# Kernel tuning notes

Measured on AMD Instinct MI355X. Metric: run time of the kernel, lower is better.

The kernel has to match this reference:

```python
import jax, jax.numpy as jnp
import numpy as np

N = 50000          # nodes
E = 800000         # edges (avg degree 16)
FEATS = [96, 96, 96, 48]


def setup_inputs() -> dict:
    key = jax.random.key(0)
    ks = jax.random.split(key, 10)
    x = jax.random.normal(ks[0], (N, FEATS[0]), dtype=jnp.float32)
    edge_index = jax.random.randint(ks[1], (2, E), 0, N, dtype=jnp.int64)
    d = {"x": x, "edge_index": edge_index}
    i = 2
    for l in range(3):
        s = 1.0 / np.sqrt(FEATS[l])
        d[f"Wl{l}"] = jax.random.uniform(ks[i], (FEATS[l], FEATS[l + 1]), jnp.float32, -s, s); i += 1
        d[f"Wr{l}"] = jax.random.uniform(ks[i], (FEATS[l], FEATS[l + 1]), jnp.float32, -s, s); i += 1
        d[f"b{l}"] = jnp.zeros((FEATS[l + 1],), jnp.float32)
    return d


def _sage_layer(h, src, dst, Wl, Wr, b, n):
    # PyG SAGEConv (aggr='mean', root_weight=True, normalize=False):
    # out_i = W_l @ mean_{j in N(i)} h_j + W_r @ h_i + b
    msg = h[src]                                                   # [E, F] gather
    ssum = jax.ops.segment_sum(msg, dst, num_segments=n)           # [N, F] scatter-add
    cnt = jax.ops.segment_sum(jnp.ones((src.shape[0], 1), h.dtype), dst, num_segments=n)
    mean = ssum / jnp.maximum(cnt, 1.0)
    return mean @ Wl + h @ Wr + b


def reference(x, edge_index, Wl0, Wr0, b0, Wl1, Wr1, b1, Wl2, Wr2, b2):
    src, dst = edge_index[0], edge_index[1]
    n = x.shape[0]
    # block = SAGEConv -> ReLU -> dropout(identity in eval)
    h = jax.nn.relu(_sage_layer(x, src, dst, Wl0, Wr0, b0, n))
    h = jax.nn.relu(_sage_layer(h, src, dst, Wl1, Wr1, b1, n))
    h = jax.nn.relu(_sage_layer(h, src, dst, Wl2, Wr2, b2, n))
    return h
```

## Files before the change

### kernel.cpp

```cpp
#include <hip/hip_runtime.h>


#define NNODES 50000
#define ZROW   50000
#define NEDGES 800000
#define CAP    64
#define LSTR   72
#define NBKT   512
#define BKSZ   98
#define NBKB   511
#define EBA    400
#define EPBA   2000
#define SEGC   20
#define CVT_N8 600000
#define CB 1172
#define WTN 46080
#define WB 90

typedef __attribute__((ext_vector_type(8))) short bf16x8;
typedef __attribute__((ext_vector_type(4))) float f32x4;

__device__ inline unsigned short f2bf(float f) {
    unsigned int u = __float_as_uint(f);
    unsigned int r = (u + 0x7fffu + ((u >> 16) & 1u)) >> 16;
    return (unsigned short)r;
}
__device__ inline float bf2f_lo(unsigned int u) { return __uint_as_float(u << 16); }
__device__ inline float bf2f_hi(unsigned int u) { return __uint_as_float(u & 0xffff0000u); }

__global__ __launch_bounds__(512) void build_a(
        const int* __restrict__ src, const int* __restrict__ dst,
        unsigned int* __restrict__ region, unsigned char* __restrict__ cnta,
        const float* __restrict__ x, unsigned short* __restrict__ h0b,
        const float* __restrict__ Wl0, const float* __restrict__ Wr0,
        const float* __restrict__ Wl1, const float* __restrict__ Wr1,
        const float* __restrict__ Wl2, const float* __restrict__ Wr2,
        unsigned short* __restrict__ WT0, unsigned short* __restrict__ WT1,
        unsigned short* __restrict__ WT2) {
    int b = blockIdx.x;
    if (b < EBA) {
        __shared__ int hist[NBKT];
        const int t = threadIdx.x;
        for (int k = t; k < NBKT; k += 512) hist[k] = 0;
        __syncthreads();
        const int e0 = b * EPBA;
        for (int i = t; i < EPBA; i += 512) {
            int d = dst[e0 + i];
            int s = src[e0 + i];
            unsigned int bk = (unsigned int)d / 98u;
            unsigned int rel = (unsigned int)d - bk * 98u;
            unsigned int val = (rel << 16) | (unsigned int)s;
            int r = atomicAdd(&hist[bk], 1);
            if (r < SEGC) region[((size_t)b * NBKT + bk) * SEGC + r] = val;
        }
        __syncthreads();
        for (int k = t; k < NBKT; k += 512)
            cnta[(size_t)k * EBA + b] = (unsigned char)min(hist[k], SEGC);
    } else if (b < EBA + CB) {
        long long t = (long long)(b - EBA) * 512 + threadIdx.x;
        if (t < CVT_N8) {
            const float4* p = reinterpret_cast<const float4*>(x + t * 8);
            float4 a = p[0], c = p[1];
            uint4 o;
            o.x = (unsigned)f2bf(a.x) | ((unsigned)f2bf(a.y) << 16);
            o.y = (unsigned)f2bf(a.z) | ((unsigned)f2bf(a.w) << 16);
            o.z = (unsigned)f2bf(c.x) | ((unsigned)f2bf(c.y) << 16);
            o.w = (unsigned)f2bf(c.z) | ((unsigned)f2bf(c.w) << 16);
            *reinterpret_cast<uint4*>(h0b + t * 8) = o;
        }
    } else if (b < EBA + CB + WB) {
        int t = (b - EBA - CB) * 512 + threadIdx.x;
        if (t >= WTN) return;
        const float* Wl; const float* Wr; unsigned short* WT; int fout; int u;
        if (t < 18432)      { Wl = Wl0; Wr = Wr0; WT = WT0; fout = 96; u = t; }
        else if (t < 36864) { Wl = Wl1; Wr = Wr1; WT = WT1; fout = 96; u = t - 18432; }
        else                { Wl = Wl2; Wr = Wr2; WT = WT2; fout = 48; u = t - 36864; }
        int j = u / 192;
        int k = u - j * 192;
        float v = (k < 96) ? Wl[k * fout + j] : Wr[(k - 96) * fout + j];
        WT[u] = f2bf(v);
    } else {
        int t = threadIdx.x;
        if (t < 12) {
            uint4 z = make_uint4(0, 0, 0, 0);
            *reinterpret_cast<uint4*>(h0b + (size_t)ZROW * 96 + t * 8) = z;
        }
    }
}

__global__ __launch_bounds__(512) void build_b(const unsigned int* __restrict__ region,
                                               const unsigned char* __restrict__ cnta,
                                               int* __restrict__ deg,
                                               unsigned short* __restrict__ colu) {
    __shared__ unsigned char cnt_l[EBA];
    __shared__ int deg_l[BKSZ];
    __shared__ __attribute__((aligned(16))) unsigned short colu_l[BKSZ * CAP];
    const int k = blockIdx.x;
    const int t = threadIdx.x;
    const int base_node = k * BKSZ;
    const int nn = min(BKSZ, NNODES - base_node);
    for (int i = t; i < EBA; i += 512) cnt_l[i] = cnta[(size_t)k * EBA + i];
    if (t < BKSZ) deg_l[t] = 0;
    __syncthreads();

    for (int cb = t; cb < EBA; cb += 512) {
        const int c = cnt_l[cb];
        const unsigned int* cell = region + ((size_t)cb * NBKT + k) * SEGC;
        for (int j = 0; j < c; j += 4) {
            uint4 q = *reinterpret_cast<const uint4*>(cell + j);
            unsigned int qq0 = q.x, qq1 = q.y, qq2 = q.z, qq3 = q.w;
            if (j + 0 < c) {
                int local = (int)(qq0 >> 16);
                int r = atomicAdd(&deg_l[local], 1);
                if (r < CAP) colu_l[local * CAP + r] = (unsigned short)(qq0 & 0xffffu);
            }
            if (j + 1 < c) {
                int local = (int)(qq1 >> 16);
                int r = atomicAdd(&deg_l[local], 1);
                if (r < CAP) colu_l[local * CAP + r] = (unsigned short)(qq1 & 0xffffu);
            }
            if (j + 2 < c) {
                int local = (int)(qq2 >> 16);
                int r = atomicAdd(&deg_l[local], 1);
                if (r < CAP) colu_l[local * CAP + r] = (unsigned short)(qq2 & 0xffffu);
            }
            if (j + 3 < c) {
                int local = (int)(qq3 >> 16);
                int r = atomicAdd(&deg_l[local], 1);
                if (r < CAP) colu_l[local * CAP + r] = (unsigned short)(qq3 & 0xffffu);
            }
        }
    }
    __syncthreads();

    for (int i = t; i < nn * (CAP / 8); i += 512) {
        *reinterpret_cast<uint4*>(colu + (size_t)base_node * CAP + i * 8) =
            *reinterpret_cast<const uint4*>(colu_l + i * 8);
    }
    if (t < nn) deg[base_node + t] = deg_l[t];
}

template <int NT, bool WRITE_BF16>
__global__ __launch_bounds__(256) void fused_layer(
    const unsigned short* __restrict__ hb,
    const int* __restrict__ deg, const unsigned short* __restrict__ colu,
    const unsigned short* __restrict__ WT,
    const float* __restrict__ bias,
    unsigned short* __restrict__ out_bf, float* __restrict__ out_f) {
    __shared__ unsigned short Asm[16][200];
    __shared__ unsigned short cols[16 * LSTR];
    const int i0 = blockIdx.x * 16;
    const int t = threadIdx.x;

    if (WRITE_BF16 && blockIdx.x == 0 && t < 12) {
        uint4 z = make_uint4(0, 0, 0, 0);
        *reinterpret_cast<uint4*>(out_bf + (size_t)ZROW * 96 + t * 8) = z;
    }

    {
        int u4 = t * 4;
        int node = u4 >> 6;
        int slot = u4 & 63;
        uint2 v = *reinterpret_cast<const uint2*>(colu + (size_t)(i0 + node) * CAP + slot);
        int d = deg[i0 + node];
        unsigned int s0 = (slot + 0 < d) ? (v.x & 0xffffu) : ZROW;
        unsigned int s1 = (slot + 1 < d) ? (v.x >> 16)     : ZROW;
        unsigned int s2 = (slot + 2 < d) ? (v.y & 0xffffu) : ZROW;
        unsigned int s3 = (slot + 3 < d) ? (v.y >> 16)     : ZROW;
        uint2 o;
        o.x = s0 | (s1 << 16);
        o.y = s2 | (s3 << 16);
        *reinterpret_cast<uint2*>(&cols[node * LSTR + slot]) = o;
    }
    __syncthreads();

    if (t < 192) {
        const int nl = t / 12;
        const int c = (t - nl * 12) * 8;
        const int d = deg[i0 + nl];
        const int d8 = d & ~7;
        const int pd4 = (d + 3) & ~3;
        float a0 = 0.f, a1 = 0.f, a2 = 0.f, a3 = 0.f, a4 = 0.f, a5 = 0.f, a6 = 0.f, a7 = 0.f;
        int j = 0;
        for (; j < d8; j += 8) {
            uint4 cu = *reinterpret_cast<const uint4*>(&cols[nl * LSTR + j]);
            int s0 = (int)(cu.x & 0xffffu), s1 = (int)(cu.x >> 16);
            int s2 = (int)(cu.y & 0xffffu), s3 = (int)(cu.y >> 16);
            int s4 = (int)(cu.z & 0xffffu), s5 = (int)(cu.z >> 16);
            int s6 = (int)(cu.w & 0xffffu), s7 = (int)(cu.w >> 16);
            uint4 u0 = *reinterpret_cast<const uint4*>(hb + (size_t)s0 * 96 + c);
            uint4 u1 = *reinterpret_cast<const uint4*>(hb + (size_t)s1 * 96 + c);
            uint4 u2 = *reinterpret_cast<const uint4*>(hb + (size_t)s2 * 96 + c);
            uint4 u3 = *reinterpret_cast<const uint4*>(hb + (size_t)s3 * 96 + c);
            uint4 u4 = *reinterpret_cast<const uint4*>(hb + (size_t)s4 * 96 + c);
            uint4 u5 = *reinterpret_cast<const uint4*>(hb + (size_t)s5 * 96 + c);
            uint4 u6 = *reinterpret_cast<const uint4*>(hb + (size_t)s6 * 96 + c);
            uint4 u7 = *reinterpret_cast<const uint4*>(hb + (size_t)s7 * 96 + c);
            a0 += bf2f_lo(u0.x) + bf2f_lo(u1.x) + bf2f_lo(u2.x) + bf2f_lo(u3.x)
                + bf2f_lo(u4.x) + bf2f_lo(u5.x) + bf2f_lo(u6.x) + bf2f_lo(u7.x);
            a1 += bf2f_hi(u0.x) + bf2f_hi(u1.x) + bf2f_hi(u2.x) + bf2f_hi(u3.x)
                + bf2f_hi(u4.x) + bf2f_hi(u5.x) + bf2f_hi(u6.x) + bf2f_hi(u7.x);
            a2 += bf2f_lo(u0.y) + bf2f_lo(u1.y) + bf2f_lo(u2.y) + bf2f_lo(u3.y)
                + bf2f_lo(u4.y) + bf2f_lo(u5.y) + bf2f_lo(u6.y) + bf2f_lo(u7.y);
            a3 += bf2f_hi(u0.y) + bf2f_hi(u1.y) + bf2f_hi(u2.y) + bf2f_hi(u3.y)
                + bf2f_hi(u4.y) + bf2f_hi(u5.y) + bf2f_hi(u6.y) + bf2f_hi(u7.y);
            a4 += bf2f_lo(u0.z) + bf2f_lo(u1.z) + bf2f_lo(u2.z) + bf2f_lo(u3.z)
                + bf2f_lo(u4.z) + bf2f_lo(u5.z) + bf2f_lo(u6.z) + bf2f_lo(u7.z);
            a5 += bf2f_hi(u0.z) + bf2f_hi(u1.z) + bf2f_hi(u2.z) + bf2f_hi(u3.z)
                + bf2f_hi(u4.z) + bf2f_hi(u5.z) + bf2f_hi(u6.z) + bf2f_hi(u7.z);
            a6 += bf2f_lo(u0.w) + bf2f_lo(u1.w) + bf2f_lo(u2.w) + bf2f_lo(u3.w)
                + bf2f_lo(u4.w) + bf2f_lo(u5.w) + bf2f_lo(u6.w) + bf2f_lo(u7.w);
            a7 += bf2f_hi(u0.w) + bf2f_hi(u1.w) + bf2f_hi(u2.w) + bf2f_hi(u3.w)
                + bf2f_hi(u4.w) + bf2f_hi(u5.w) + bf2f_hi(u6.w) + bf2f_hi(u7.w);
        }
        for (; j < pd4; j += 4) {
            uint2 cu = *reinterpret_cast<const uint2*>(&cols[nl * LSTR + j]);
            int s0 = (int)(cu.x & 0xffffu), s1 = (int)(cu.x >> 16);
            int s2 = (int)(cu.y & 0xffffu), s3 = (int)(cu.y >> 16);
            uint4 u0 = *reinterpret_cast<const uint4*>(hb + (size_t)s0 * 96 + c);
            uint4 u1 = *reinterpret_cast<const uint4*>(hb + (size_t)s1 * 96 + c);
            uint4 u2 = *reinterpret_cast<const uint4*>(hb + (size_t)s2 * 96 + c);
            uint4 u3 = *reinterpret_cast<const uint4*>(hb + (size_t)s3 * 96 + c);
            a0 += bf2f_lo(u0.x) + bf2f_lo(u1.x) + bf2f_lo(u2.x) + bf2f_lo(u3.x);
            a1 += bf2f_hi(u0.x) + bf2f_hi(u1.x) + bf2f_hi(u2.x) + bf2f_hi(u3.x);
            a2 += bf2f_lo(u0.y) + bf2f_lo(u1.y) + bf2f_lo(u2.y) + bf2f_lo(u3.y);
            a3 += bf2f_hi(u0.y) + bf2f_hi(u1.y) + bf2f_hi(u2.y) + bf2f_hi(u3.y);
            a4 += bf2f_lo(u0.z) + bf2f_lo(u1.z) + bf2f_lo(u2.z) + bf2f_lo(u3.z);
            a5 += bf2f_hi(u0.z) + bf2f_hi(u1.z) + bf2f_hi(u2.z) + bf2f_hi(u3.z);
            a6 += bf2f_lo(u0.w) + bf2f_lo(u1.w) + bf2f_lo(u2.w) + bf2f_lo(u3.w);
            a7 += bf2f_hi(u0.w) + bf2f_hi(u1.w) + bf2f_hi(u2.w) + bf2f_hi(u3.w);
        }
        float inv = (d > 0) ? 1.0f / (float)d : 0.0f;
        uint4 o;
        o.x = (unsigned)f2bf(a0 * inv) | ((unsigned)f2bf(a1 * inv) << 16);
        o.y = (unsigned)f2bf(a2 * inv) | ((unsigned)f2bf(a3 * inv) << 16);
        o.z = (unsigned)f2bf(a4 * inv) | ((unsigned)f2bf(a5 * inv) << 16);
        o.w = (unsigned)f2bf(a6 * inv) | ((unsigned)f2bf(a7 * inv) << 16);
        *reinterpret_cast<uint4*>(&Asm[nl][c]) = o;
    }
    __syncthreads();

    const int wave = t >> 6;
    const int lane = t & 63;
    const int m = lane & 15;
    const int kq = (lane >> 4) * 8;

    bf16x8 afr[6];
#pragma unroll
    for (int kk = 0; kk < 3; ++kk)
        afr[kk] = *reinterpret_cast<const bf16x8*>(&Asm[m][kq + kk * 32]);
    const unsigned short* hrow = hb + (size_t)(i0 + m) * 96 + kq;
#pragma unroll
    for (int kk = 0; kk < 3; ++kk)
        afr[3 + kk] = *reinterpret_cast<const bf16x8*>(hrow + kk * 32);

    const int r0 = (lane >> 4) * 4;
    for (int nt = wave; nt < NT; nt += 4) {
        f32x4 acc = {0.f, 0.f, 0.f, 0.f};
        const unsigned short* wrow = WT + (size_t)(nt * 16 + m) * 192 + kq;
#pragma unroll
        for (int kk = 0; kk < 6; ++kk) {
            bf16x8 bfr = *reinterpret_cast<const bf16x8*>(wrow + kk * 32);
            acc = __builtin_amdgcn_mfma_f32_16x16x32_bf16(afr[kk], bfr, acc, 0, 0, 0);
        }
        int colj = nt * 16 + m;
        float bv = bias[colj];
#pragma unroll
        for (int r = 0; r < 4; ++r) {
            float v = fmaxf(acc[r] + bv, 0.0f);
            size_t oi = (size_t)(i0 + r0 + r) * (16 * NT) + colj;
            if (WRITE_BF16) out_bf[oi] = f2bf(v);
            else            out_f[oi] = v;
        }
    }
}

extern "C" void kernel_launch(void* const* d_in, const int* in_sizes, int n_in,
                              void* d_out, int out_size, void* d_ws, size_t ws_size,
                              hipStream_t stream) {
    const float* x   = (const float*)d_in[0];
    const int*   ei  = (const int*)d_in[1];
    const float* Wl0 = (const float*)d_in[2];
    const float* Wr0 = (const float*)d_in[3];
    const float* b0  = (const float*)d_in[4];
    const float* Wl1 = (const float*)d_in[5];
    const float* Wr1 = (const float*)d_in[6];
    const float* b1  = (const float*)d_in[7];
    const float* Wl2 = (const float*)d_in[8];
    const float* Wr2 = (const float*)d_in[9];
    const float* b2  = (const float*)d_in[10];
    float* out = (float*)d_out;

    const int* src = ei;
    const int* dst = ei + NEDGES;

    char* p = (char*)d_ws;
    int* deg = (int*)p;                        p += (size_t)50176 * 4;
    unsigned short* colu = (unsigned short*)p; p += (size_t)50176 * CAP * 2;
    unsigned char* cnta = (unsigned char*)p;   p += (size_t)NBKT * EBA;
    unsigned short* WT0 = (unsigned short*)p;  p += 96 * 192 * 2;
    unsigned short* WT1 = (unsigned short*)p;  p += 96 * 192 * 2;
    unsigned short* WT2 = (unsigned short*)p;  p += 48 * 192 * 2;
    unsigned short* h0b = (unsigned short*)p;  p += (size_t)(NNODES + 1) * 96 * 2 + 64;
    unsigned short* h1b = (unsigned short*)p;  p += (size_t)(NNODES + 1) * 96 * 2 + 64;
    unsigned short* h2b = (unsigned short*)p;  p += (size_t)(NNODES + 1) * 96 * 2 + 64;

    unsigned int* region = (unsigned int*)h1b;

    build_a<<<EBA + CB + WB + 1, 512, 0, stream>>>(
        src, dst, region, cnta, x, h0b,
        Wl0, Wr0, Wl1, Wr1, Wl2, Wr2, WT0, WT1, WT2);

    build_b<<<NBKB, 512, 0, stream>>>(region, cnta, deg, colu);

    const int LB = NNODES / 16;
    fused_layer<6, true><<<LB, 256, 0, stream>>>(h0b, deg, colu, WT0, b0, h1b, nullptr);
    fused_layer<6, true><<<LB, 256, 0, stream>>>(h1b, deg, colu, WT1, b1, h2b, nullptr);
    fused_layer<3, false><<<LB, 256, 0, stream>>>(h2b, deg, colu, WT2, b2, nullptr, out);
}
```

Measured before the change: 195.4 us.

## Project last layer before aggregation to gather 48-wide features instead of 96

Uses linearity of mean aggregation to apply Wl2 to h2 inside the layer-1 epilogue, writing a 48-wide bf16 Y2 array. The final kernel then gathers and averages the narrower projected features and adds the root term plus bias. This halves gather traffic in the last layer. In exchange it adds an extra barrier and a small MFMA in layer 1, and the projected values are rounded to bf16 before averaging.

```diff
diff --git a/kernel.cpp b/kernel.cpp
--- a/kernel.cpp
+++ b/kernel.cpp
@@ -36,7 +36,7 @@
         const float* __restrict__ Wl1, const float* __restrict__ Wr1,
         const float* __restrict__ Wl2, const float* __restrict__ Wr2,
         unsigned short* __restrict__ WT0, unsigned short* __restrict__ WT1,
-        unsigned short* __restrict__ WT2) {
+        unsigned short* __restrict__ WT2l, unsigned short* __restrict__ WT2r) {
     int b = blockIdx.x;
     if (b < EBA) {
         __shared__ int hist[NBKT];
@@ -71,14 +71,21 @@
     } else if (b < EBA + CB + WB) {
         int t = (b - EBA - CB) * 512 + threadIdx.x;
         if (t >= WTN) return;
-        const float* Wl; const float* Wr; unsigned short* WT; int fout; int u;
-        if (t < 18432)      { Wl = Wl0; Wr = Wr0; WT = WT0; fout = 96; u = t; }
-        else if (t < 36864) { Wl = Wl1; Wr = Wr1; WT = WT1; fout = 96; u = t - 18432; }
-        else                { Wl = Wl2; Wr = Wr2; WT = WT2; fout = 48; u = t - 36864; }
-        int j = u / 192;
-        int k = u - j * 192;
-        float v = (k < 96) ? Wl[k * fout + j] : Wr[(k - 96) * fout + j];
-        WT[u] = f2bf(v);
+        if (t < 18432) {
+            int u = t; int j = u / 192; int k = u - j * 192;
+            float v = (k < 96) ? Wl0[k * 96 + j] : Wr0[(k - 96) * 96 + j];
+            WT0[u] = f2bf(v);
+        } else if (t < 36864) {
+            int u = t - 18432; int j = u / 192; int k = u - j * 192;
+            float v = (k < 96) ? Wl1[k * 96 + j] : Wr1[(k - 96) * 96 + j];
+            WT1[u] = f2bf(v);
+        } else if (t < 41472) {
+            int u = t - 36864; int j = u / 96; int k = u - j * 96;
+            WT2l[u] = f2bf(Wl2[k * 48 + j]);
+        } else {
+            int u = t - 41472; int j = u / 96; int k = u - j * 96;
+            WT2r[u] = f2bf(Wr2[k * 48 + j]);
+        }
     } else {
         int t = threadIdx.x;
         if (t < 12) {
@@ -140,21 +147,29 @@
     if (t < nn) deg[base_node + t] = deg_l[t];
 }
 
-template <int NT, bool WRITE_BF16>
+template <int NT, bool Y2EP>
 __global__ __launch_bounds__(256) void fused_layer(
     const unsigned short* __restrict__ hb,
     const int* __restrict__ deg, const unsigned short* __restrict__ colu,
     const unsigned short* __restrict__ WT,
     const float* __restrict__ bias,
-    unsigned short* __restrict__ out_bf, float* __restrict__ out_f) {
+    unsigned short* __restrict__ out_bf,
+    const unsigned short* __restrict__ WT2l,
+    unsigned short* __restrict__ Y2b) {
     __shared__ unsigned short Asm[16][200];
     __shared__ unsigned short cols[16 * LSTR];
     const int i0 = blockIdx.x * 16;
     const int t = threadIdx.x;
 
-    if (WRITE_BF16 && blockIdx.x == 0 && t < 12) {
-        uint4 z = make_uint4(0, 0, 0, 0);
-        *reinterpret_cast<uint4*>(out_bf + (size_t)ZROW * 96 + t * 8) = z;
+    if (blockIdx.x == 0) {
+        if (t < 12) {
+            uint4 z = make_uint4(0, 0, 0, 0);
+            *reinterpret_cast<uint4*>(out_bf + (size_t)ZROW * 96 + t * 8) = z;
+        }
+        if (Y2EP && t >= 16 && t < 22) {
+            uint4 z = make_uint4(0, 0, 0, 0);
+            *reinterpret_cast<uint4*>(Y2b + (size_t)ZROW * 48 + (t - 16) * 8) = z;
+        }
     }
 
     {
@@ -254,6 +269,8 @@
     for (int kk = 0; kk < 3; ++kk)
         afr[3 + kk] = *reinterpret_cast<const bf16x8*>(hrow + kk * 32);
 
+    if (Y2EP) __syncthreads();
+
     const int r0 = (lane >> 4) * 4;
     for (int nt = wave; nt < NT; nt += 4) {
         f32x4 acc = {0.f, 0.f, 0.f, 0.f};
@@ -268,9 +285,153 @@
 #pragma unroll
         for (int r = 0; r < 4; ++r) {
             float v = fmaxf(acc[r] + bv, 0.0f);
-            size_t oi = (size_t)(i0 + r0 + r) * (16 * NT) + colj;
-            if (WRITE_BF16) out_bf[oi] = f2bf(v);
-            else            out_f[oi] = v;
+            unsigned short hv = f2bf(v);
+            out_bf[(size_t)(i0 + r0 + r) * (16 * NT) + colj] = hv;
+            if (Y2EP) Asm[r0 + r][colj] = hv;
+        }
+    }
+
+    if (Y2EP) {
+        __syncthreads();
+        if (wave < 3) {
+            bf16x8 a2[3];
+#pragma unroll
+            for (int kk = 0; kk < 3; ++kk)
+                a2[kk] = *reinterpret_cast<const bf16x8*>(&Asm[m][kq + kk * 32]);
+            f32x4 acc = {0.f, 0.f, 0.f, 0.f};
+            const unsigned short* wrow = WT2l + (size_t)(wave * 16 + m) * 96 + kq;
+#pragma unroll
+            for (int kk = 0; kk < 3; ++kk) {
+                bf16x8 bfr = *reinterpret_cast<const bf16x8*>(wrow + kk * 32);
+                acc = __builtin_amdgcn_mfma_f32_16x16x32_bf16(a2[kk], bfr, acc, 0, 0, 0);
+            }
+            int colj2 = wave * 16 + m;
+#pragma unroll
+            for (int r = 0; r < 4; ++r)
+                Y2b[(size_t)(i0 + r0 + r) * 48 + colj2] = f2bf(acc[r]);
+        }
+    }
+}
+
+__global__ __launch_bounds__(256) void fused_final(
+    const unsigned short* __restrict__ hb,
+    const unsigned short* __restrict__ Y2b,
+    const int* __restrict__ deg, const unsigned short* __restrict__ colu,
+    const unsigned short* __restrict__ WT2r,
+    const float* __restrict__ bias,
+    float* __restrict__ out_f) {
+    __shared__ float Msm[16][56];
+    __shared__ unsigned short cols[16 * LSTR];
+    const int i0 = blockIdx.x * 16;
+    const int t = threadIdx.x;
+
+    {
+        int u4 = t * 4;
+        int node = u4 >> 6;
+        int slot = u4 & 63;
+        uint2 v = *reinterpret_cast<const uint2*>(colu + (size_t)(i0 + node) * CAP + slot);
+        int d = deg[i0 + node];
+        unsigned int s0 = (slot + 0 < d) ? (v.x & 0xffffu) : ZROW;
+        unsigned int s1 = (slot + 1 < d) ? (v.x >> 16)     : ZROW;
+        unsigned int s2 = (slot + 2 < d) ? (v.y & 0xffffu) : ZROW;
+        unsigned int s3 = (slot + 3 < d) ? (v.y >> 16)     : ZROW;
+        uint2 o;
+        o.x = s0 | (s1 << 16);
+        o.y = s2 | (s3 << 16);
+        *reinterpret_cast<uint2*>(&cols[node * LSTR + slot]) = o;
+    }
+    __syncthreads();
+
+    if (t < 96) {
+        const int nl = t / 6;
+        const int c = (t - nl * 6) * 8;
+        const int d = deg[i0 + nl];
+        const int d8 = d & ~7;
+        const int pd4 = (d + 3) & ~3;
+        float a0 = 0.f, a1 = 0.f, a2 = 0.f, a3 = 0.f, a4 = 0.f, a5 = 0.f, a6 = 0.f, a7 = 0.f;
+        int j = 0;
+        for (; j < d8; j += 8) {
+            uint4 cu = *reinterpret_cast<const uint4*>(&cols[nl * LSTR + j]);
+            int s0 = (int)(cu.x & 0xffffu), s1 = (int)(cu.x >> 16);
+            int s2 = (int)(cu.y & 0xffffu), s3 = (int)(cu.y >> 16);
+            int s4 = (int)(cu.z & 0xffffu), s5 = (int)(cu.z >> 16);
+            int s6 = (int)(cu.w & 0xffffu), s7 = (int)(cu.w >> 16);
+            uint4 u0 = *reinterpret_cast<const uint4*>(Y2b + (size_t)s0 * 48 + c);
+            uint4 u1 = *reinterpret_cast<const uint4*>(Y2b + (size_t)s1 * 48 + c);
+            uint4 u2 = *reinterpret_cast<const uint4*>(Y2b + (size_t)s2 * 48 + c);
+            uint4 u3 = *reinterpret_cast<const uint4*>(Y2b + (size_t)s3 * 48 + c);
+            uint4 u4 = *reinterpret_cast<const uint4*>(Y2b + (size_t)s4 * 48 + c);
+            uint4 u5 = *reinterpret_cast<const uint4*>(Y2b + (size_t)s5 * 48 + c);
+            uint4 u6 = *reinterpret_cast<const uint4*>(Y2b + (size_t)s6 * 48 + c);
+            uint4 u7 = *reinterpret_cast<const uint4*>(Y2b + (size_t)s7 * 48 + c);
+            a0 += bf2f_lo(u0.x) + bf2f_lo(u1.x) + bf2f_lo(u2.x) + bf2f_lo(u3.x)
+                + bf2f_lo(u4.x) + bf2f_lo(u5.x) + bf2f_lo(u6.x) + bf2f_lo(u7.x);
+            a1 += bf2f_hi(u0.x) + bf2f_hi(u1.x) + bf2f_hi(u2.x) + bf2f_hi(u3.x)
+                + bf2f_hi(u4.x) + bf2f_hi(u5.x) + bf2f_hi(u6.x) + bf2f_hi(u7.x);
+            a2 += bf2f_lo(u0.y) + bf2f_lo(u1.y) + bf2f_lo(u2.y) + bf2f_lo(u3.y)
+                + bf2f_lo(u4.y) + bf2f_lo(u5.y) + bf2f_lo(u6.y) + bf2f_lo(u7.y);
+            a3 += bf2f_hi(u0.y) + bf2f_hi(u1.y) + bf2f_hi(u2.y) + bf2f_hi(u3.y)
+                + bf2f_hi(u4.y) + bf2f_hi(u5.y) + bf2f_hi(u6.y) + bf2f_hi(u7.y);
+            a4 += bf2f_lo(u0.z) + bf2f_lo(u1.z) + bf2f_lo(u2.z) + bf2f_lo(u3.z)
+                + bf2f_lo(u4.z) + bf2f_lo(u5.z) + bf2f_lo(u6.z) + bf2f_lo(u7.z);
+            a5 += bf2f_hi(u0.z) + bf2f_hi(u1.z) + bf2f_hi(u2.z) + bf2f_hi(u3.z)
+                + bf2f_hi(u4.z) + bf2f_hi(u5.z) + bf2f_hi(u6.z) + bf2f_hi(u7.z);
+            a6 += bf2f_lo(u0.w) + bf2f_lo(u1.w) + bf2f_lo(u2.w) + bf2f_lo(u3.w)
+                + bf2f_lo(u4.w) + bf2f_lo(u5.w) + bf2f_lo(u6.w) + bf2f_lo(u7.w);
+            a7 += bf2f_hi(u0.w) + bf2f_hi(u1.w) + bf2f_hi(u2.w) + bf2f_hi(u3.w)
+                + bf2f_hi(u4.w) + bf2f_hi(u5.w) + bf2f_hi(u6.w) + bf2f_hi(u7.w);
+        }
+        for (; j < pd4; j += 4) {
+            uint2 cu = *reinterpret_cast<const uint2*>(&cols[nl * LSTR + j]);
+            int s0 = (int)(cu.x & 0xffffu), s1 = (int)(cu.x >> 16);
+            int s2 = (int)(cu.y & 0xffffu), s3 = (int)(cu.y >> 16);
+            uint4 u0 = *reinterpret_cast<const uint4*>(Y2b + (size_t)s0 * 48 + c);
+            uint4 u1 = *reinterpret_cast<const uint4*>(Y2b + (size_t)s1 * 48 + c);
+            uint4 u2 = *reinterpret_cast<const uint4*>(Y2b + (size_t)s2 * 48 + c);
+            uint4 u3 = *reinterpret_cast<const uint4*>(Y2b + (size_t)s3 * 48 + c);
+            a0 += bf2f_lo(u0.x) + bf2f_lo(u1.x) + bf2f_lo(u2.x) + bf2f_lo(u3.x);
+            a1 += bf2f_hi(u0.x) + bf2f_hi(u1.x) + bf2f_hi(u2.x) + bf2f_hi(u3.x);
+            a2 += bf2f_lo(u0.y) + bf2f_lo(u1.y) + bf2f_lo(u2.y) + bf2f_lo(u3.y);
+            a3 += bf2f_hi(u0.y) + bf2f_hi(u1.y) + bf2f_hi(u2.y) + bf2f_hi(u3.y);
+            a4 += bf2f_lo(u0.z) + bf2f_lo(u1.z) + bf2f_lo(u2.z) + bf2f_lo(u3.z);
+            a5 += bf2f_hi(u0.z) + bf2f_hi(u1.z) + bf2f_hi(u2.z) + bf2f_hi(u3.z);
+            a6 += bf2f_lo(u0.w) + bf2f_lo(u1.w) + bf2f_lo(u2.w) + bf2f_lo(u3.w);
+            a7 += bf2f_hi(u0.w) + bf2f_hi(u1.w) + bf2f_hi(u2.w) + bf2f_hi(u3.w);
+        }
+        float inv = (d > 0) ? 1.0f / (float)d : 0.0f;
+        float4 o0 = make_float4(a0 * inv, a1 * inv, a2 * inv, a3 * inv);
+        float4 o1 = make_float4(a4 * inv, a5 * inv, a6 * inv, a7 * inv);
+        *reinterpret_cast<float4*>(&Msm[nl][c]) = o0;
+        *reinterpret_cast<float4*>(&Msm[nl][c + 4]) = o1;
+    }
+    __syncthreads();
+
+    const int wave = t >> 6;
+    const int lane = t & 63;
+    const int m = lane & 15;
+    const int kq = (lane >> 4) * 8;
+    const int r0 = (lane >> 4) * 4;
+
+    if (wave < 3) {
+        bf16x8 afr[3];
+        const unsigned short* hrow = hb + (size_t)(i0 + m) * 96 + kq;
+#pragma unroll
+        for (int kk = 0; kk < 3; ++kk)
+            afr[kk] = *reinterpret_cast<const bf16x8*>(hrow + kk * 32);
+        f32x4 acc = {0.f, 0.f, 0.f, 0.f};
+        const unsigned short* wrow = WT2r + (size_t)(wave * 16 + m) * 96 + kq;
+#pragma unroll
+        for (int kk = 0; kk < 3; ++kk) {
+            bf16x8 bfr = *reinterpret_cast<const bf16x8*>(wrow + kk * 32);
+            acc = __builtin_amdgcn_mfma_f32_16x16x32_bf16(afr[kk], bfr, acc, 0, 0, 0);
+        }
+        int colj = wave * 16 + m;
+        float bv = bias[colj];
+#pragma unroll
+        for (int r = 0; r < 4; ++r) {
+            int row = r0 + r;
+            float v = fmaxf(acc[r] + Msm[row][colj] + bv, 0.0f);
+            out_f[(size_t)(i0 + row) * 48 + colj] = v;
         }
     }
 }
@@ -300,21 +461,25 @@
     unsigned char* cnta = (unsigned char*)p;   p += (size_t)NBKT * EBA;
     unsigned short* WT0 = (unsigned short*)p;  p += 96 * 192 * 2;
     unsigned short* WT1 = (unsigned short*)p;  p += 96 * 192 * 2;
-    unsigned short* WT2 = (unsigned short*)p;  p += 48 * 192 * 2;
+    unsigned short* WT2l = (unsigned short*)p; p += 48 * 96 * 2;
+    unsigned short* WT2r = (unsigned short*)p; p += 48 * 96 * 2;
     unsigned short* h0b = (unsigned short*)p;  p += (size_t)(NNODES + 1) * 96 * 2 + 64;
     unsigned short* h1b = (unsigned short*)p;  p += (size_t)(NNODES + 1) * 96 * 2 + 64;
     unsigned short* h2b = (unsigned short*)p;  p += (size_t)(NNODES + 1) * 96 * 2 + 64;
+    unsigned short* Y2b = (unsigned short*)p;  p += (size_t)(NNODES + 1) * 48 * 2 + 64;
 
     unsigned int* region = (unsigned int*)h1b;
 
     build_a<<<EBA + CB + WB + 1, 512, 0, stream>>>(
         src, dst, region, cnta, x, h0b,
-        Wl0, Wr0, Wl1, Wr1, Wl2, Wr2, WT0, WT1, WT2);
+        Wl0, Wr0, Wl1, Wr1, Wl2, Wr2, WT0, WT1, WT2l, WT2r);
 
     build_b<<<NBKB, 512, 0, stream>>>(region, cnta, deg, colu);
 
     const int LB = NNODES / 16;
-    fused_layer<6, true><<<LB, 256, 0, stream>>>(h0b, deg, colu, WT0, b0, h1b, nullptr);
-    fused_layer<6, true><<<LB, 256, 0, stream>>>(h1b, deg, colu, WT1, b1, h2b, nullptr);
-    fused_layer<3, false><<<LB, 256, 0, stream>>>(h2b, deg, colu, WT2, b2, nullptr, out);
-}
+    fused_layer<6, false><<<LB, 256, 0, stream>>>(h0b, deg, colu, WT0, b0, h1b,
+                                                  nullptr, nullptr);
+    fused_layer<6, true><<<LB, 256, 0, stream>>>(h1b, deg, colu, WT1, b1, h2b,
+                                                 WT2l, Y2b);
+    fused_final<<<LB, 256, 0, stream>>>(h2b, Y2b, deg, colu, WT2r, b2, out);
+}
```

Measured after the change: 190.3 us (median of 2 runs). -2.6%, faster.
